# Kernel optimization log

Hardware: AMD Instinct MI355X
Metric: run time of the kernel (lower is better)

## Reference

```python
import jax, jax.numpy as jnp
import numpy as np

BZ, N_STEPS, D_IN, D_HID, D_OUT = 4096, 128, 32, 128, 32


def setup_inputs() -> dict:
    key = jax.random.key(0)
    ks = jax.random.split(key, 16)
    g = lambda k, s: jax.random.normal(k, s, dtype=jnp.float32) * 0.05
    return {
        "fcn_latent": g(ks[0], (BZ, D_IN)),
        "encoder_outputs": g(ks[1], (BZ, N_STEPS, D_HID)),
        "att1_w": g(ks[2], (D_IN, 2 * D_IN)),
        "att1_b": g(ks[3], (D_IN,)),
        "att2_w": g(ks[4], (D_HID, 2 * D_HID)),
        "att2_b": g(ks[5], (D_HID,)),
        "gru1_wih": g(ks[6], (3 * D_HID, D_IN)),
        "gru1_whh": g(ks[7], (3 * D_HID, D_HID)),
        "gru1_bih": g(ks[8], (3 * D_HID,)),
        "gru1_bhh": g(ks[9], (3 * D_HID,)),
        "gru2_wih": g(ks[10], (3 * D_HID, D_HID)),
        "gru2_whh": g(ks[11], (3 * D_HID, D_HID)),
        "gru2_bih": g(ks[12], (3 * D_HID,)),
        "gru2_bhh": g(ks[13], (3 * D_HID,)),
        "out_w": g(ks[14], (D_OUT, D_HID)),
        "out_b": g(ks[15], (D_OUT,)),
    }


def _gru_cell(x, h, w_ih, w_hh, b_ih, b_hh):
    # torch.nn.GRUCell math: gates ordered (r, z, n)
    gi = x @ w_ih.T + b_ih
    gh = h @ w_hh.T + b_hh
    i_r, i_z, i_n = jnp.split(gi, 3, axis=-1)
    h_r, h_z, h_n = jnp.split(gh, 3, axis=-1)
    r = jax.nn.sigmoid(i_r + h_r)
    z = jax.nn.sigmoid(i_z + h_z)
    n = jnp.tanh(i_n + r * h_n)
    return (1.0 - z) * n + z * h


def _attend(h, enc_t, w, b):
    # h: (bz, D), enc_t: (bz, d_enc). Faithful to original (mixes batch into contraction).
    scores = h.T @ enc_t                     # (D, d_enc)
    weight = jax.nn.softmax(scores, axis=-1)
    context = (weight @ enc_t.T).T           # (bz, D)
    return jnp.tanh(jnp.concatenate([context, h], axis=1) @ w.T + b)


def reference(fcn_latent, encoder_outputs, att1_w, att1_b, att2_w, att2_b,
              gru1_wih, gru1_whh, gru1_bih, gru1_bhh,
              gru2_wih, gru2_whh, gru2_bih, gru2_bhh, out_w, out_b):
    # step 0: attention over d_input-sized hidden, then GRUCell(d_input -> d_hidden)
    att0 = _attend(fcn_latent, encoder_outputs[:, 0, :], att1_w, att1_b)
    h_rep = jnp.tile(fcn_latent, (1, D_HID // D_IN))          # (bz, d_hidden)
    h = _gru_cell(att0, h_rep, gru1_wih, gru1_whh, gru1_bih, gru1_bhh)

    def step(h, enc_t):
        a = _attend(h, enc_t, att2_w, att2_b)
        h2 = _gru_cell(a, h, gru2_wih, gru2_whh, gru2_bih, gru2_bhh)
        return h2, h2

    enc_rest = jnp.swapaxes(encoder_outputs[:, 1:, :], 0, 1)  # (n_steps-1, bz, d_hidden)
    _, hs_rest = jax.lax.scan(step, h, enc_rest)
    collector = jnp.concatenate([h[:, None, :], jnp.swapaxes(hs_rest, 0, 1)], axis=1)
    reconstruction = collector @ out_w.T + out_b              # (bz, n_steps, d_output)
    return reconstruction
```

## Files before the change

### kernel.cpp

```cpp
#include <hip/hip_runtime.h>
#include <math.h>

#define BZ 4096
#define NT 128
#define DH 128
#define DI 32
#define LDW 132
#define SCR_KS 2116
#define SA 136
#define ST 40

typedef short bf16x8 __attribute__((ext_vector_type(8)));
typedef float f32x4 __attribute__((ext_vector_type(4)));

__device__ __forceinline__ float4 ld4(const float* p) { return *(const float4*)(p); }
__device__ __forceinline__ void st4(float* p, float4 v) { *(float4*)(p) = v; }
__device__ __forceinline__ float dot4(float4 w, float4 a) {
  return w.x*a.x + w.y*a.y + w.z*a.z + w.w*a.w;
}
__device__ __forceinline__ float sigm(float x) { return 1.f / (1.f + expf(-x)); }
__device__ __forceinline__ unsigned short f2b(float x) {
  unsigned u = __float_as_uint(x);
  u += 0x7FFFu + ((u >> 16) & 1u);
  return (unsigned short)(u >> 16);
}

__global__ __launch_bounds__(512) void k_prep(const float* __restrict__ a2w,
                                              const float* __restrict__ wih,
                                              const float* __restrict__ whh,
                                              const float* __restrict__ outw,
                                              unsigned short* __restrict__ wbf) {
  const int idx = blockIdx.x * 512 + threadIdx.x;
  if (idx >= 147456) return;
  const int tile = idx >> 14, pos = idx & 16383;
  float v;
  if (tile == 0)      v = a2w[(pos >> 7) * 256 + (pos & 127)];
  else if (tile == 1) v = a2w[(pos >> 7) * 256 + 128 + (pos & 127)];
  else if (tile == 2) v = wih[pos];
  else if (tile == 3) v = whh[pos];
  else if (tile == 4) v = wih[16384 + pos];
  else if (tile == 5) v = whh[16384 + pos];
  else if (tile == 6) v = wih[32768 + pos];
  else if (tile == 7) v = whh[32768 + pos];
  else                v = (pos < 4096) ? outw[pos] : 0.f;
  wbf[idx] = f2b(v);
}

template<int D>
__global__ __launch_bounds__(512) void k_scores(const float* __restrict__ hsrc,
                                                const float* __restrict__ enc,
                                                int t, float* __restrict__ spart) {
  constexpr int IG = D / 8;
  constexpr int JC = (D == 128) ? 4 : 1;
  constexpr int HS = D + 4;
  __shared__ float hs[64 * HS];
  __shared__ float es[64 * LDW];
  const int p = blockIdx.x, tid = threadIdx.x, b0 = p * 64;
  for (int idx = tid; idx < 64 * (D / 4); idx += 512) {
    const int r = idx / (D / 4), c4 = (idx % (D / 4)) * 4;
    st4(hs + r * HS + c4, ld4(hsrc + (size_t)(b0 + r) * D + c4));
  }
  for (int idx = tid; idx < 64 * 32; idx += 512) {
    const int r = idx >> 5, c4 = (idx & 31) << 2;
    st4(es + r * LDW + c4, ld4(enc + ((size_t)(b0 + r) * NT + t) * DH + c4));
  }
  __syncthreads();
  const int ig = tid % IG, jg = tid / IG;
  const int i0 = ig * 8, j0 = jg * JC;
  float acc[8][JC];
#pragma unroll
  for (int a = 0; a < 8; ++a)
#pragma unroll
    for (int b = 0; b < JC; ++b) acc[a][b] = 0.f;
  for (int b = 0; b < 64; ++b) {
    float4 h0 = ld4(hs + b * HS + i0);
    float4 h1 = ld4(hs + b * HS + i0 + 4);
    float hv[8] = {h0.x, h0.y, h0.z, h0.w, h1.x, h1.y, h1.z, h1.w};
    float ev[JC];
    if (JC == 4) {
      float4 e = ld4(es + b * LDW + j0);
      ev[0] = e.x; ev[1] = e.y; ev[2] = e.z; ev[3] = e.w;
    } else {
      ev[0] = es[b * LDW + j0];
    }
#pragma unroll
    for (int ii = 0; ii < 8; ++ii)
#pragma unroll
      for (int jj = 0; jj < JC; ++jj) acc[ii][jj] += hv[ii] * ev[jj];
  }
#pragma unroll
  for (int ii = 0; ii < 8; ++ii)
#pragma unroll
    for (int jj = 0; jj < JC; ++jj)
      spart[((size_t)p * D + (i0 + ii)) * 128 + j0 + jj] = acc[ii][jj];
}

template<int R, int P>
__global__ __launch_bounds__(128) void k_soft(const float* __restrict__ spart,
                                              float* __restrict__ W,
                                              unsigned short* __restrict__ Wmb) {
  const int r = blockIdx.x, j = threadIdx.x;
  float s = 0.f;
#pragma unroll 8
  for (int p = 0; p < P; ++p) s += spart[((size_t)p * R + r) * 128 + j];
  __shared__ float xm[2], xs[2];
  float m = s;
  for (int o = 1; o < 64; o <<= 1) m = fmaxf(m, __shfl_xor(m, o));
  if ((j & 63) == 0) xm[j >> 6] = m;
  __syncthreads();
  m = fmaxf(xm[0], xm[1]);
  float e = expf(s - m);
  float sum = e;
  for (int o = 1; o < 64; o <<= 1) sum += __shfl_xor(sum, o);
  if ((j & 63) == 0) xs[j >> 6] = sum;
  __syncthreads();
  sum = xs[0] + xs[1];
  const float val = e / sum;
  W[r * 128 + j] = val;
  Wmb[r * 128 + j] = f2b(val);
}

__global__ __launch_bounds__(128) void k_sum(const float* __restrict__ spart,
                                             float* __restrict__ S1,
                                             float* __restrict__ S2) {
  const int r = blockIdx.x, j = threadIdx.x;
  float s = 0.f;
#pragma unroll 8
  for (int p = 0; p < 64; ++p) s += spart[((size_t)p * 128 + r) * 128 + j];
  S1[r * 128 + j] = s;
  S2[r * 128 + j] = 0.f;
}

struct WTile { bf16x8 k[4]; };
struct AFrag { bf16x8 k[4]; };

__device__ __forceinline__ void loadW(WTile& wt, const unsigned short* __restrict__ base,
                                      int R, int g) {
#pragma unroll
  for (int ks = 0; ks < 4; ++ks)
    wt.k[ks] = *(const bf16x8*)(base + (size_t)R * 128 + ks * 32 + g * 8);
}
__device__ __forceinline__ void loadA(AFrag& a, const unsigned short* act, int n, int g) {
  const char* ab = (const char*)act + n * (2 * SA) + g * 16;
#pragma unroll
  for (int ks = 0; ks < 4; ++ks) a.k[ks] = *(const bf16x8*)(ab + ks * 64);
}
__device__ __forceinline__ void mmrr(f32x4& acc, const AFrag& a, const WTile& w) {
#pragma unroll
  for (int ks = 0; ks < 4; ++ks)
    acc = __builtin_amdgcn_mfma_f32_16x16x32_bf16(a.k[ks], w.k[ks], acc, 0, 0, 0);
}
__device__ __forceinline__ void mmls(f32x4& acc, const unsigned short* Wt,
                                     const unsigned short* act, int R, int n, int g) {
  const char* ab = (const char*)act + n * (2 * SA) + g * 16;
  const char* wb = (const char*)Wt;
  const int sw = (R & 7) << 4;
#pragma unroll
  for (int ks = 0; ks < 4; ++ks) {
    bf16x8 b = *(const bf16x8*)(wb + ((R * 256 + ks * 64 + g * 16) ^ sw));
    bf16x8 a = *(const bf16x8*)(ab + ks * 64);
    acc = __builtin_amdgcn_mfma_f32_16x16x32_bf16(a, b, acc, 0, 0, 0);
  }
}

__global__ __launch_bounds__(512, 2) void k_step3(
    const float* __restrict__ enc, int t, int do_next,
    const float* __restrict__ Srd, float* __restrict__ Sac, float* __restrict__ Szr,
    const unsigned short* __restrict__ wbf,
    const float* __restrict__ att2b,
    const float* __restrict__ bih, const float* __restrict__ bhh,
    float* __restrict__ hist) {
  __shared__ __align__(16) unsigned short Wslot[16384];
  __shared__ __align__(16) unsigned short el[32 * SA], hl[32 * SA];
  __shared__ __align__(16) unsigned short ctxl[32 * SA], al[32 * SA];
  __shared__ __align__(16) unsigned short hnT[128 * ST], encT[128 * ST];
  const int tid = threadIdx.x, b0 = blockIdx.x * 32;
  const int w = tid >> 6, l = tid & 63;
  const int n = l & 15, g4 = l >> 4;
  const int c = w * 16 + n;
  const f32x4 z4 = {0.f, 0.f, 0.f, 0.f};
  const float* __restrict__ hprev_g = hist + (size_t)(t - 1) * (BZ * DH);
  float* __restrict__ hcur_g = hist + (size_t)t * (BZ * DH);

  {
    const int row = tid >> 2, q = tid & 3;
    const float* sr = Srd + row * 128 + q * 32;
    float4 v[8];
    float mx = -1e30f;
#pragma unroll
    for (int i = 0; i < 8; ++i) {
      v[i] = ld4(sr + 4 * i);
      mx = fmaxf(mx, fmaxf(fmaxf(v[i].x, v[i].y), fmaxf(v[i].z, v[i].w)));
    }
    mx = fmaxf(mx, __shfl_xor(mx, 1));
    mx = fmaxf(mx, __shfl_xor(mx, 2));
    float sum = 0.f;
#pragma unroll
    for (int i = 0; i < 8; ++i) {
      v[i].x = expf(v[i].x - mx); v[i].y = expf(v[i].y - mx);
      v[i].z = expf(v[i].z - mx); v[i].w = expf(v[i].w - mx);
      sum += (v[i].x + v[i].y) + (v[i].z + v[i].w);
    }
    sum += __shfl_xor(sum, 1);
    sum += __shfl_xor(sum, 2);
    const float inv = 1.f / sum;
    char* wb = (char*)Wslot;
    const int sw = (row & 7) << 4;
#pragma unroll
    for (int ch = 0; ch < 4; ++ch) {
      unsigned short h8[8] = {
        f2b(v[2*ch].x * inv),   f2b(v[2*ch].y * inv),
        f2b(v[2*ch].z * inv),   f2b(v[2*ch].w * inv),
        f2b(v[2*ch+1].x * inv), f2b(v[2*ch+1].y * inv),
        f2b(v[2*ch+1].z * inv), f2b(v[2*ch+1].w * inv)
      };
      *(uint4*)(wb + ((row * 256 + q * 64 + ch * 16) ^ sw)) = *(const uint4*)h8;
    }
  }

  {
    const int r = tid >> 4, c8 = (tid & 15) << 3;
    float4 e0 = ld4(enc + ((size_t)(b0 + r) * NT + t) * DH + c8);
    float4 e1 = ld4(enc + ((size_t)(b0 + r) * NT + t) * DH + c8 + 4);
    float4 h0 = ld4(hprev_g + (size_t)(b0 + r) * DH + c8);
    float4 h1 = ld4(hprev_g + (size_t)(b0 + r) * DH + c8 + 4);
    unsigned short e8[8] = {f2b(e0.x), f2b(e0.y), f2b(e0.z), f2b(e0.w),
                            f2b(e1.x), f2b(e1.y), f2b(e1.z), f2b(e1.w)};
    unsigned short h8[8] = {f2b(h0.x), f2b(h0.y), f2b(h0.z), f2b(h0.w),
                            f2b(h1.x), f2b(h1.y), f2b(h1.z), f2b(h1.w)};
    *(uint4*)(el + r * SA + c8) = *(const uint4*)e8;
    *(uint4*)(hl + r * SA + c8) = *(const uint4*)h8;
  }
  if (do_next) {
    const int r = tid & 31, c8 = (tid >> 5) << 3;
    float4 e0 = ld4(enc + ((size_t)(b0 + r) * NT + t + 1) * DH + c8);
    float4 e1 = ld4(enc + ((size_t)(b0 + r) * NT + t + 1) * DH + c8 + 4);
    encT[(c8 + 0) * ST + r] = f2b(e0.x); encT[(c8 + 1) * ST + r] = f2b(e0.y);
    encT[(c8 + 2) * ST + r] = f2b(e0.z); encT[(c8 + 3) * ST + r] = f2b(e0.w);
    encT[(c8 + 4) * ST + r] = f2b(e1.x); encT[(c8 + 5) * ST + r] = f2b(e1.y);
    encT[(c8 + 6) * ST + r] = f2b(e1.z); encT[(c8 + 7) * ST + r] = f2b(e1.w);
  }
  if (do_next && tid < 128) Szr[blockIdx.x * 128 + tid] = 0.f;

  WTile wA2a, wA2b, wIR, wHR, wIZ, wHZ, wIN, wHN;
  loadW(wA2a, wbf + 0 * 16384, c, g4);
  loadW(wA2b, wbf + 1 * 16384, c, g4);
  loadW(wIR,  wbf + 2 * 16384, c, g4);
  loadW(wHR,  wbf + 3 * 16384, c, g4);
  loadW(wIZ,  wbf + 4 * 16384, c, g4);
  loadW(wHZ,  wbf + 5 * 16384, c, g4);
  loadW(wIN,  wbf + 6 * 16384, c, g4);
  loadW(wHN,  wbf + 7 * 16384, c, g4);

  float hprev[2][4];
#pragma unroll
  for (int hh = 0; hh < 2; ++hh)
#pragma unroll
    for (int j = 0; j < 4; ++j)
      hprev[hh][j] = hprev_g[(size_t)(b0 + hh * 16 + g4 * 4 + j) * DH + c];
  const float b2c = att2b[c];
  const float bihR = bih[c], bihZ = bih[DH + c], bihN = bih[2 * DH + c];
  const float bhhR = bhh[c], bhhZ = bhh[DH + c], bhhN = bhh[2 * DH + c];
  __syncthreads();

#pragma unroll
  for (int hh = 0; hh < 2; ++hh) {
    f32x4 aC = z4;
    mmls(aC, Wslot, el + hh * 16 * SA, c, n, g4);
#pragma unroll
    for (int j = 0; j < 4; ++j) ctxl[(hh * 16 + g4 * 4 + j) * SA + c] = f2b(aC[j]);
  }
  __syncthreads();
#pragma unroll
  for (int hh = 0; hh < 2; ++hh) {
    AFrag fC, fH;
    loadA(fC, ctxl + hh * 16 * SA, n, g4);
    loadA(fH, hl + hh * 16 * SA, n, g4);
    f32x4 aA = z4;
    mmrr(aA, fC, wA2a);
    mmrr(aA, fH, wA2b);
#pragma unroll
    for (int j = 0; j < 4; ++j)
      al[(hh * 16 + g4 * 4 + j) * SA + c] = f2b(tanhf(aA[j] + b2c));
  }
  __syncthreads();
  f32x4 aR[2], aZ[2], aIN[2], aHN[2];
#pragma unroll
  for (int hh = 0; hh < 2; ++hh) {
    AFrag fA, fH;
    loadA(fA, al + hh * 16 * SA, n, g4);
    loadA(fH, hl + hh * 16 * SA, n, g4);
    f32x4 tr_ = z4, tz = z4, ti = z4, th = z4;
    mmrr(tr_, fA, wIR); mmrr(tr_, fH, wHR);
    mmrr(tz, fA, wIZ);  mmrr(tz, fH, wHZ);
    mmrr(ti, fA, wIN);  mmrr(th, fH, wHN);
    aR[hh] = tr_; aZ[hh] = tz; aIN[hh] = ti; aHN[hh] = th;
  }
#pragma unroll
  for (int hh = 0; hh < 2; ++hh) {
#pragma unroll
    for (int j = 0; j < 4; ++j) {
      const int row = hh * 16 + g4 * 4 + j;
      const float rg = sigm(aR[hh][j] + bihR + bhhR);
      const float zg = sigm(aZ[hh][j] + bihZ + bhhZ);
      const float ng = tanhf(aIN[hh][j] + bihN + rg * (aHN[hh][j] + bhhN));
      const float hv = (1.f - zg) * ng + zg * hprev[hh][j];
      hnT[c * ST + row] = f2b(hv);
      hcur_g[(size_t)(b0 + row) * DH + c] = hv;
    }
  }
  if (!do_next) return;
  __syncthreads();
  {
    bf16x8 afr = *(const bf16x8*)(hnT + (16 * w + n) * ST + g4 * 8);
    float* Sn = Sac + (size_t)(16 * w + g4 * 4) * 128 + n;
#pragma unroll
    for (int nt = 0; nt < 8; ++nt) {
      bf16x8 bfr = *(const bf16x8*)(encT + (16 * nt + n) * ST + g4 * 8);
      f32x4 s = __builtin_amdgcn_mfma_f32_16x16x32_bf16(afr, bfr, z4, 0, 0, 0);
#pragma unroll
      for (int jj = 0; jj < 4; ++jj) atomicAdd(Sn + jj * 128 + nt * 16, s[jj]);
    }
  }
}

__global__ __launch_bounds__(256) void k_out(const float* __restrict__ hist,
                                             const float* __restrict__ outw,
                                             const float* __restrict__ outb,
                                             float* __restrict__ out) {
  __shared__ float wl[32 * 132];
  __shared__ float bl[32];
  const int tid = threadIdx.x;
  for (int idx = tid; idx < 32 * 32; idx += 256) {
    const int r = idx >> 5, c4 = (idx & 31) << 2;
    st4(wl + r * 132 + c4, ld4(outw + r * 128 + c4));
  }
  if (tid < 32) bl[tid] = outb[tid];
  __syncthreads();
  const int rlocal = tid >> 2, q = tid & 3;
  const size_t ri = (size_t)blockIdx.x * 64 + rlocal;
  const int b = (int)(ri & 4095), t = 1 + (int)(ri >> 12);
  const float* hr = hist + (size_t)t * (BZ * DH) + (size_t)b * DH + q * 32;
  float4 hv[8];
#pragma unroll
  for (int i = 0; i < 8; ++i) hv[i] = ld4(hr + 4 * i);
  float acc[32];
#pragma unroll
  for (int o = 0; o < 32; ++o) {
    const float* wr = wl + o * 132 + q * 32;
    float a = 0.f;
#pragma unroll
    for (int i = 0; i < 8; ++i) a += dot4(ld4(wr + 4 * i), hv[i]);
    acc[o] = a;
  }
#pragma unroll
  for (int o = 0; o < 32; ++o) {
    acc[o] += __shfl_xor(acc[o], 1);
    acc[o] += __shfl_xor(acc[o], 2);
  }
  float* op = out + ((size_t)b * NT + t) * DI;
#pragma unroll
  for (int oo = 0; oo < 8; ++oo) {
    const int o = q * 8 + oo;
    op[o] = acc[o] + bl[o];
  }
}

__device__ __forceinline__ void stage128(float* dst, const float* __restrict__ src,
                                         int rows, int srcStride, int tid) {
  const int n4 = rows * 32;
  for (int idx = tid; idx < n4; idx += 512) {
    const int r = idx >> 5, c4 = (idx & 31) << 2;
    st4(dst + r * LDW + c4, ld4(src + (size_t)r * srcStride + c4));
  }
}
template<int ADD>
__device__ __forceinline__ void phase128(float* Wb, const float* act, float* dest, int tid) {
  const int ks = tid & 7, cg_ = (tid >> 3) & 15, r4 = tid >> 7;
  const int rbase = r4 * 4;
  float acc[4][8];
#pragma unroll
  for (int a = 0; a < 4; ++a)
#pragma unroll
    for (int b = 0; b < 8; ++b) acc[a][b] = 0.f;
#pragma unroll
  for (int ch = 0; ch < 4; ++ch) {
    const int k = ks * 4 + ch * 32;
    float4 av[4];
#pragma unroll
    for (int ri = 0; ri < 4; ++ri) av[ri] = ld4(act + (rbase + ri) * LDW + k);
#pragma unroll
    for (int i = 0; i < 8; ++i) {
      float4 wv = ld4(Wb + (cg_ * 8 + i) * LDW + k);
#pragma unroll
      for (int ri = 0; ri < 4; ++ri) acc[ri][i] += dot4(wv, av[ri]);
    }
  }
  __syncthreads();
#pragma unroll
  for (int ri = 0; ri < 4; ++ri) {
    st4(Wb + ks * SCR_KS + (rbase + ri) * LDW + cg_ * 8,
        make_float4(acc[ri][0], acc[ri][1], acc[ri][2], acc[ri][3]));
    st4(Wb + ks * SCR_KS + (rbase + ri) * LDW + cg_ * 8 + 4,
        make_float4(acc[ri][4], acc[ri][5], acc[ri][6], acc[ri][7]));
  }
  __syncthreads();
  const int fr = tid >> 5, fc = (tid & 31) << 2;
  float4 s = make_float4(0.f, 0.f, 0.f, 0.f);
#pragma unroll
  for (int kk = 0; kk < 8; ++kk) {
    float4 v = ld4(Wb + kk * SCR_KS + fr * LDW + fc);
    s.x += v.x; s.y += v.y; s.z += v.z; s.w += v.w;
  }
  float* dp = dest + fr * LDW + fc;
  if (ADD) { float4 o = ld4(dp); s.x += o.x; s.y += o.y; s.z += o.z; s.w += o.w; }
  st4(dp, s);
  __syncthreads();
}
__device__ __forceinline__ void gru_out(float p0, float p1, float p2, float p3,
                                        float bi0, float bi1, float bi2,
                                        float bh0, float bh1, float bh2,
                                        float hv, float* o) {
  const float rg = sigm(p0 + bi0 + bh0);
  const float zg = sigm(p1 + bi1 + bh1);
  const float ng = tanhf(p2 + bi2 + rg * (p3 + bh2));
  *o = (1.f - zg) * ng + zg * hv;
}
__global__ __launch_bounds__(512) void k_main0(
    const float* __restrict__ enc, const float* __restrict__ fcn,
    const float* __restrict__ W0,
    const float* __restrict__ A1, const float* __restrict__ b1,
    const float* __restrict__ wih, const float* __restrict__ whh,
    const float* __restrict__ bih, const float* __restrict__ bhh,
    const float* __restrict__ outw, const float* __restrict__ outb,
    float* __restrict__ h, float* __restrict__ out) {
  __shared__ float Wb[16960];
  __shared__ float el[16 * LDW], hrep[16 * LDW], al[16 * LDW], hn[16 * LDW];
  __shared__ float pre[4][16 * LDW];
  __shared__ float fl[16 * 36];
  const int tid = threadIdx.x, b0 = blockIdx.x * 16;
  {
    const int r = tid >> 5, c4 = (tid & 31) << 2;
    st4(el + r * LDW + c4, ld4(enc + ((size_t)(b0 + r) * NT + 0) * DH + c4));
  }
  {
    const int r = tid >> 5, cc = tid & 31;
    fl[r * 36 + cc] = fcn[(size_t)(b0 + r) * DI + cc];
  }
  __syncthreads();
  {
    const int r = tid >> 5, fc = (tid & 31) << 2;
    st4(hrep + r * LDW + fc, ld4(fl + r * 36 + (fc & 31)));
  }
  stage128(Wb, W0, 32, 128, tid);
  __syncthreads();
  {
    const int r = tid >> 5, q = tid & 31;
    float acc = 0.f;
#pragma unroll 8
    for (int k4 = 0; k4 < 32; ++k4)
      acc += dot4(ld4(Wb + q * LDW + k4 * 4), ld4(el + r * LDW + k4 * 4));
    hn[r * LDW + q] = acc;
  }
  __syncthreads();
  for (int idx = tid; idx < 512; idx += 512) {
    const int r = idx >> 4, c4 = (idx & 15) << 2;
    st4(Wb + r * 68 + c4, ld4(A1 + r * 64 + c4));
  }
  __syncthreads();
  {
    const int r = tid >> 5, i = tid & 31;
    float acc = b1[i];
#pragma unroll
    for (int k4 = 0; k4 < 8; ++k4)
      acc += dot4(ld4(Wb + i * 68 + k4 * 4), ld4(hn + r * LDW + k4 * 4));
#pragma unroll
    for (int k4 = 0; k4 < 8; ++k4)
      acc += dot4(ld4(Wb + i * 68 + 32 + k4 * 4), ld4(fl + r * 36 + k4 * 4));
    al[r * LDW + i] = tanhf(acc);
  }
  __syncthreads();
  for (int idx = tid; idx < 384 * 8; idx += 512) {
    const int r = idx >> 3, c4 = (idx & 7) << 2;
    st4(Wb + r * 36 + c4, ld4(wih + r * 32 + c4));
  }
  __syncthreads();
  {
    const int r = tid >> 5, ccc = tid & 31;
#pragma unroll
    for (int m = 0; m < 12; ++m) {
      const int cc = ccc + 32 * m, g = cc >> 7, col = cc & 127;
      float acc = 0.f;
#pragma unroll
      for (int k4 = 0; k4 < 8; ++k4)
        acc += dot4(ld4(Wb + cc * 36 + k4 * 4), ld4(al + r * LDW + k4 * 4));
      pre[(g == 2) ? 2 : g][r * LDW + col] = acc;
    }
  }
  __syncthreads();
  stage128(Wb, whh, 128, 128, tid);          __syncthreads();
  phase128<1>(Wb, hrep, pre[0], tid);
  stage128(Wb, whh + 16384, 128, 128, tid);  __syncthreads();
  phase128<1>(Wb, hrep, pre[1], tid);
  stage128(Wb, whh + 32768, 128, 128, tid);  __syncthreads();
  phase128<0>(Wb, hrep, pre[3], tid);
  {
    const int fr = tid >> 5, fc = (tid & 31) << 2;
    float4 p0 = ld4(&pre[0][fr * LDW + fc]), p1 = ld4(&pre[1][fr * LDW + fc]);
    float4 p2 = ld4(&pre[2][fr * LDW + fc]), p3 = ld4(&pre[3][fr * LDW + fc]);
    float4 bi0 = ld4(bih + fc), bi1 = ld4(bih + DH + fc), bi2 = ld4(bih + 2 * DH + fc);
    float4 bh0 = ld4(bhh + fc), bh1 = ld4(bhh + DH + fc), bh2 = ld4(bhh + 2 * DH + fc);
    float4 hv = ld4(hrep + fr * LDW + fc);
    float o0, o1, o2, o3;
    gru_out(p0.x, p1.x, p2.x, p3.x, bi0.x, bi1.x, bi2.x, bh0.x, bh1.x, bh2.x, hv.x, &o0);
    gru_out(p0.y, p1.y, p2.y, p3.y, bi0.y, bi1.y, bi2.y, bh0.y, bh1.y, bh2.y, hv.y, &o1);
    gru_out(p0.z, p1.z, p2.z, p3.z, bi0.z, bi1.z, bi2.z, bh0.z, bh1.z, bh2.z, hv.z, &o2);
    gru_out(p0.w, p1.w, p2.w, p3.w, bi0.w, bi1.w, bi2.w, bh0.w, bh1.w, bh2.w, hv.w, &o3);
    float4 hnew = make_float4(o0, o1, o2, o3);
    st4(hn + fr * LDW + fc, hnew);
    st4(h + (size_t)(b0 + fr) * DH + fc, hnew);
  }
  __syncthreads();
  stage128(Wb, outw, 32, 128, tid);
  __syncthreads();
  {
    const int r = tid >> 5, cc = tid & 31;
    float acc = outb[cc];
#pragma unroll 8
    for (int k4 = 0; k4 < 32; ++k4)
      acc += dot4(ld4(Wb + cc * LDW + k4 * 4), ld4(hn + r * LDW + k4 * 4));
    out[((size_t)(b0 + r) * NT + 0) * DI + cc] = acc;
  }
}

extern "C" void kernel_launch(void* const* d_in, const int* in_sizes, int n_in,
                              void* d_out, int out_size, void* d_ws, size_t ws_size,
                              hipStream_t stream) {
  (void)in_sizes; (void)n_in; (void)out_size; (void)ws_size;
  const float* fcn  = (const float*)d_in[0];
  const float* enc  = (const float*)d_in[1];
  const float* a1w  = (const float*)d_in[2];
  const float* a1b  = (const float*)d_in[3];
  const float* a2w  = (const float*)d_in[4];
  const float* a2b  = (const float*)d_in[5];
  const float* w1ih = (const float*)d_in[6];
  const float* w1hh = (const float*)d_in[7];
  const float* b1ih = (const float*)d_in[8];
  const float* b1hh = (const float*)d_in[9];
  const float* w2ih = (const float*)d_in[10];
  const float* w2hh = (const float*)d_in[11];
  const float* b2ih = (const float*)d_in[12];
  const float* b2hh = (const float*)d_in[13];
  const float* outw = (const float*)d_in[14];
  const float* outb = (const float*)d_in[15];
  float* out = (float*)d_out;
  float* ws  = (float*)d_ws;

  float* spart = ws;
  float* Wbuf  = ws + 1048576;
  float* Sbuf  = ws + 1064960;
  unsigned short* wbf = (unsigned short*)(ws + 1130496);
  unsigned short* Wmb = (unsigned short*)(ws + 1204224);
  float* hist  = ws + 1310720;

  k_prep<<<288, 512, 0, stream>>>(a2w, w2ih, w2hh, outw, wbf);

  k_scores<DI><<<64, 512, 0, stream>>>(fcn, enc, 0, spart);
  k_soft<DI, 64><<<DI, 128, 0, stream>>>(spart, Wbuf, Wmb);
  k_main0<<<BZ / 16, 512, 0, stream>>>(enc, fcn, Wbuf, a1w, a1b,
                                       w1ih, w1hh, b1ih, b1hh, outw, outb, hist, out);
  k_scores<DH><<<64, 512, 0, stream>>>(hist, enc, 1, spart);
  k_sum<<<128, 128, 0, stream>>>(spart, Sbuf + 16384, Sbuf + 2 * 16384);

  for (int t = 1; t < NT; ++t) {
    const int do_next = (t < NT - 1) ? 1 : 0;
    const float* Srd = Sbuf + (size_t)(t & 3) * 16384;
    float* Sac = Sbuf + (size_t)((t + 1) & 3) * 16384;
    float* Szr = Sbuf + (size_t)((t + 2) & 3) * 16384;
    k_step3<<<128, 512, 0, stream>>>(enc, t, do_next, Srd, Sac, Szr, wbf, a2b,
                                     b2ih, b2hh, hist);
  }
  k_out<<<(BZ * (NT - 1)) / 64, 256, 0, stream>>>(hist, outw, outb, out);
}
```

Baseline: 3.246 ms.

## Halve step blocks to 64 rows each and fuse output projection into step kernel

```diff
diff --git a/kernel.cpp b/kernel.cpp
--- a/kernel.cpp
+++ b/kernel.cpp
@@ -8,7 +8,7 @@
 #define LDW 132
 #define SCR_KS 2116
 #define SA 136
-#define ST 40
+#define ST2 72
 
 typedef short bf16x8 __attribute__((ext_vector_type(8)));
 typedef float f32x4 __attribute__((ext_vector_type(4)));
@@ -169,12 +169,47 @@
     const unsigned short* __restrict__ wbf,
     const float* __restrict__ att2b,
     const float* __restrict__ bih, const float* __restrict__ bhh,
-    float* __restrict__ hist) {
+    const float* __restrict__ outw, const float* __restrict__ outb,
+    float* __restrict__ hist, float* __restrict__ out) {
   __shared__ __align__(16) unsigned short Wslot[16384];
-  __shared__ __align__(16) unsigned short el[32 * SA], hl[32 * SA];
-  __shared__ __align__(16) unsigned short ctxl[32 * SA], al[32 * SA];
-  __shared__ __align__(16) unsigned short hnT[128 * ST], encT[128 * ST];
-  const int tid = threadIdx.x, b0 = blockIdx.x * 32;
+  __shared__ __align__(16) unsigned short el[64 * SA], hl[64 * SA];
+  __shared__ __align__(16) unsigned short ctxl[64 * SA], al[64 * SA];
+  __shared__ __align__(16) unsigned short hnT[128 * ST2], encT[128 * ST2];
+  const int tid = threadIdx.x;
+
+  if (blockIdx.x >= 64) {
+    if (t < 2) return;
+    const int rl = tid >> 2, q = tid & 3;
+    const int b = (blockIdx.x - 64) * 128 + rl;
+    const int tt = t - 1;
+    const float* hr = hist + (size_t)tt * (BZ * DH) + (size_t)b * DH + q * 32;
+    float4 hv[8];
+#pragma unroll
+    for (int i = 0; i < 8; ++i) hv[i] = ld4(hr + 4 * i);
+    float acc[32];
+#pragma unroll
+    for (int o = 0; o < 32; ++o) {
+      const float* wr = outw + o * 128 + q * 32;
+      float a = 0.f;
+#pragma unroll
+      for (int i = 0; i < 8; ++i) a += dot4(ld4(wr + 4 * i), hv[i]);
+      acc[o] = a;
+    }
+#pragma unroll
+    for (int o = 0; o < 32; ++o) {
+      acc[o] += __shfl_xor(acc[o], 1);
+      acc[o] += __shfl_xor(acc[o], 2);
+    }
+    float* op = out + ((size_t)b * NT + tt) * DI;
+#pragma unroll
+    for (int oo = 0; oo < 8; ++oo) {
+      const int o = q * 8 + oo;
+      op[o] = acc[o] + outb[o];
+    }
+    return;
+  }
+
+  const int b0 = blockIdx.x * 64;
   const int w = tid >> 6, l = tid & 63;
   const int n = l & 15, g4 = l >> 4;
   const int c = w * 16 + n;
@@ -219,28 +254,34 @@
   }
 
   {
-    const int r = tid >> 4, c8 = (tid & 15) << 3;
-    float4 e0 = ld4(enc + ((size_t)(b0 + r) * NT + t) * DH + c8);
-    float4 e1 = ld4(enc + ((size_t)(b0 + r) * NT + t) * DH + c8 + 4);
-    float4 h0 = ld4(hprev_g + (size_t)(b0 + r) * DH + c8);
-    float4 h1 = ld4(hprev_g + (size_t)(b0 + r) * DH + c8 + 4);
-    unsigned short e8[8] = {f2b(e0.x), f2b(e0.y), f2b(e0.z), f2b(e0.w),
-                            f2b(e1.x), f2b(e1.y), f2b(e1.z), f2b(e1.w)};
-    unsigned short h8[8] = {f2b(h0.x), f2b(h0.y), f2b(h0.z), f2b(h0.w),
-                            f2b(h1.x), f2b(h1.y), f2b(h1.z), f2b(h1.w)};
-    *(uint4*)(el + r * SA + c8) = *(const uint4*)e8;
-    *(uint4*)(hl + r * SA + c8) = *(const uint4*)h8;
+    const int r = tid >> 3, cc = (tid & 7) << 4;
+    const float* ep = enc + ((size_t)(b0 + r) * NT + t) * DH + cc;
+    const float* hp = hprev_g + (size_t)(b0 + r) * DH + cc;
+    float4 e0 = ld4(ep), e1 = ld4(ep + 4), e2 = ld4(ep + 8), e3 = ld4(ep + 12);
+    float4 h0 = ld4(hp), h1 = ld4(hp + 4), h2 = ld4(hp + 8), h3 = ld4(hp + 12);
+    unsigned short e8a[8] = {f2b(e0.x), f2b(e0.y), f2b(e0.z), f2b(e0.w),
+                             f2b(e1.x), f2b(e1.y), f2b(e1.z), f2b(e1.w)};
+    unsigned short e8b[8] = {f2b(e2.x), f2b(e2.y), f2b(e2.z), f2b(e2.w),
+                             f2b(e3.x), f2b(e3.y), f2b(e3.z), f2b(e3.w)};
+    unsigned short h8a[8] = {f2b(h0.x), f2b(h0.y), f2b(h0.z), f2b(h0.w),
+                             f2b(h1.x), f2b(h1.y), f2b(h1.z), f2b(h1.w)};
+    unsigned short h8b[8] = {f2b(h2.x), f2b(h2.y), f2b(h2.z), f2b(h2.w),
+                             f2b(h3.x), f2b(h3.y), f2b(h3.z), f2b(h3.w)};
+    *(uint4*)(el + r * SA + cc) = *(const uint4*)e8a;
+    *(uint4*)(el + r * SA + cc + 8) = *(const uint4*)e8b;
+    *(uint4*)(hl + r * SA + cc) = *(const uint4*)h8a;
+    *(uint4*)(hl + r * SA + cc + 8) = *(const uint4*)h8b;
   }
   if (do_next) {
-    const int r = tid & 31, c8 = (tid >> 5) << 3;
-    float4 e0 = ld4(enc + ((size_t)(b0 + r) * NT + t + 1) * DH + c8);
-    float4 e1 = ld4(enc + ((size_t)(b0 + r) * NT + t + 1) * DH + c8 + 4);
-    encT[(c8 + 0) * ST + r] = f2b(e0.x); encT[(c8 + 1) * ST + r] = f2b(e0.y);
-    encT[(c8 + 2) * ST + r] = f2b(e0.z); encT[(c8 + 3) * ST + r] = f2b(e0.w);
-    encT[(c8 + 4) * ST + r] = f2b(e1.x); encT[(c8 + 5) * ST + r] = f2b(e1.y);
-    encT[(c8 + 6) * ST + r] = f2b(e1.z); encT[(c8 + 7) * ST + r] = f2b(e1.w);
-  }
-  if (do_next && tid < 128) Szr[blockIdx.x * 128 + tid] = 0.f;
+    const int r = tid & 63, c16 = (tid >> 6) << 4;
+    const float* ep = enc + ((size_t)(b0 + r) * NT + t + 1) * DH + c16;
+    float4 v0 = ld4(ep), v1 = ld4(ep + 4), v2 = ld4(ep + 8), v3 = ld4(ep + 12);
+    const float vv[16] = {v0.x, v0.y, v0.z, v0.w, v1.x, v1.y, v1.z, v1.w,
+                          v2.x, v2.y, v2.z, v2.w, v3.x, v3.y, v3.z, v3.w};
+#pragma unroll
+    for (int k = 0; k < 16; ++k) encT[(c16 + k) * ST2 + r] = f2b(vv[k]);
+    if (tid < 256) Szr[blockIdx.x * 256 + tid] = 0.f;
+  }
 
   WTile wA2a, wA2b, wIR, wHR, wIZ, wHZ, wIN, wHN;
   loadW(wA2a, wbf + 0 * 16384, c, g4);
@@ -252,9 +293,9 @@
   loadW(wIN,  wbf + 6 * 16384, c, g4);
   loadW(wHN,  wbf + 7 * 16384, c, g4);
 
-  float hprev[2][4];
-#pragma unroll
-  for (int hh = 0; hh < 2; ++hh)
+  float hprev[4][4];
+#pragma unroll
+  for (int hh = 0; hh < 4; ++hh)
 #pragma unroll
     for (int j = 0; j < 4; ++j)
       hprev[hh][j] = hprev_g[(size_t)(b0 + hh * 16 + g4 * 4 + j) * DH + c];
@@ -264,7 +305,7 @@
   __syncthreads();
 
 #pragma unroll
-  for (int hh = 0; hh < 2; ++hh) {
+  for (int hh = 0; hh < 4; ++hh) {
     f32x4 aC = z4;
     mmls(aC, Wslot, el + hh * 16 * SA, c, n, g4);
 #pragma unroll
@@ -272,7 +313,7 @@
   }
   __syncthreads();
 #pragma unroll
-  for (int hh = 0; hh < 2; ++hh) {
+  for (int hh = 0; hh < 4; ++hh) {
     AFrag fC, fH;
     loadA(fC, ctxl + hh * 16 * SA, n, g4);
     loadA(fH, hl + hh * 16 * SA, n, g4);
@@ -284,9 +325,8 @@
       al[(hh * 16 + g4 * 4 + j) * SA + c] = f2b(tanhf(aA[j] + b2c));
   }
   __syncthreads();
-  f32x4 aR[2], aZ[2], aIN[2], aHN[2];
-#pragma unroll
-  for (int hh = 0; hh < 2; ++hh) {
+#pragma unroll
+  for (int hh = 0; hh < 4; ++hh) {
     AFrag fA, fH;
     loadA(fA, al + hh * 16 * SA, n, g4);
     loadA(fH, hl + hh * 16 * SA, n, g4);
@@ -294,30 +334,29 @@
     mmrr(tr_, fA, wIR); mmrr(tr_, fH, wHR);
     mmrr(tz, fA, wIZ);  mmrr(tz, fH, wHZ);
     mmrr(ti, fA, wIN);  mmrr(th, fH, wHN);
-    aR[hh] = tr_; aZ[hh] = tz; aIN[hh] = ti; aHN[hh] = th;
-  }
-#pragma unroll
-  for (int hh = 0; hh < 2; ++hh) {
 #pragma unroll
     for (int j = 0; j < 4; ++j) {
       const int row = hh * 16 + g4 * 4 + j;
-      const float rg = sigm(aR[hh][j] + bihR + bhhR);
-      const float zg = sigm(aZ[hh][j] + bihZ + bhhZ);
-      const float ng = tanhf(aIN[hh][j] + bihN + rg * (aHN[hh][j] + bhhN));
+      const float rg = sigm(tr_[j] + bihR + bhhR);
+      const float zg = sigm(tz[j] + bihZ + bhhZ);
+      const float ng = tanhf(ti[j] + bihN + rg * (th[j] + bhhN));
       const float hv = (1.f - zg) * ng + zg * hprev[hh][j];
-      hnT[c * ST + row] = f2b(hv);
+      hnT[c * ST2 + row] = f2b(hv);
       hcur_g[(size_t)(b0 + row) * DH + c] = hv;
     }
   }
   if (!do_next) return;
   __syncthreads();
   {
-    bf16x8 afr = *(const bf16x8*)(hnT + (16 * w + n) * ST + g4 * 8);
+    bf16x8 afr0 = *(const bf16x8*)(hnT + (16 * w + n) * ST2 + g4 * 8);
+    bf16x8 afr1 = *(const bf16x8*)(hnT + (16 * w + n) * ST2 + 32 + g4 * 8);
     float* Sn = Sac + (size_t)(16 * w + g4 * 4) * 128 + n;
 #pragma unroll
     for (int nt = 0; nt < 8; ++nt) {
-      bf16x8 bfr = *(const bf16x8*)(encT + (16 * nt + n) * ST + g4 * 8);
-      f32x4 s = __builtin_amdgcn_mfma_f32_16x16x32_bf16(afr, bfr, z4, 0, 0, 0);
+      bf16x8 bfr0 = *(const bf16x8*)(encT + (16 * nt + n) * ST2 + g4 * 8);
+      bf16x8 bfr1 = *(const bf16x8*)(encT + (16 * nt + n) * ST2 + 32 + g4 * 8);
+      f32x4 s = __builtin_amdgcn_mfma_f32_16x16x32_bf16(afr0, bfr0, z4, 0, 0, 0);
+      s = __builtin_amdgcn_mfma_f32_16x16x32_bf16(afr1, bfr1, s, 0, 0, 0);
 #pragma unroll
       for (int jj = 0; jj < 4; ++jj) atomicAdd(Sn + jj * 128 + nt * 16, s[jj]);
     }
@@ -327,19 +366,10 @@
 __global__ __launch_bounds__(256) void k_out(const float* __restrict__ hist,
                                              const float* __restrict__ outw,
                                              const float* __restrict__ outb,
-                                             float* __restrict__ out) {
-  __shared__ float wl[32 * 132];
-  __shared__ float bl[32];
+                                             float* __restrict__ out, int t) {
   const int tid = threadIdx.x;
-  for (int idx = tid; idx < 32 * 32; idx += 256) {
-    const int r = idx >> 5, c4 = (idx & 31) << 2;
-    st4(wl + r * 132 + c4, ld4(outw + r * 128 + c4));
-  }
-  if (tid < 32) bl[tid] = outb[tid];
-  __syncthreads();
-  const int rlocal = tid >> 2, q = tid & 3;
-  const size_t ri = (size_t)blockIdx.x * 64 + rlocal;
-  const int b = (int)(ri & 4095), t = 1 + (int)(ri >> 12);
+  const int rl = tid >> 2, q = tid & 3;
+  const int b = blockIdx.x * 64 + rl;
   const float* hr = hist + (size_t)t * (BZ * DH) + (size_t)b * DH + q * 32;
   float4 hv[8];
 #pragma unroll
@@ -347,7 +377,7 @@
   float acc[32];
 #pragma unroll
   for (int o = 0; o < 32; ++o) {
-    const float* wr = wl + o * 132 + q * 32;
+    const float* wr = outw + o * 128 + q * 32;
     float a = 0.f;
 #pragma unroll
     for (int i = 0; i < 8; ++i) a += dot4(ld4(wr + 4 * i), hv[i]);
@@ -362,7 +392,7 @@
 #pragma unroll
   for (int oo = 0; oo < 8; ++oo) {
     const int o = q * 8 + oo;
-    op[o] = acc[o] + bl[o];
+    op[o] = acc[o] + outb[o];
   }
 }
 
@@ -577,8 +607,8 @@
     const float* Srd = Sbuf + (size_t)(t & 3) * 16384;
     float* Sac = Sbuf + (size_t)((t + 1) & 3) * 16384;
     float* Szr = Sbuf + (size_t)((t + 2) & 3) * 16384;
-    k_step3<<<128, 512, 0, stream>>>(enc, t, do_next, Srd, Sac, Szr, wbf, a2b,
-                                     b2ih, b2hh, hist);
-  }
-  k_out<<<(BZ * (NT - 1)) / 64, 256, 0, stream>>>(hist, outw, outb, out);
-}
+    k_step3<<<96, 512, 0, stream>>>(enc, t, do_next, Srd, Sac, Szr, wbf, a2b,
+                                    b2ih, b2hh, outw, outb, hist, out);
+  }
+  k_out<<<64, 256, 0, stream>>>(hist, outw, outb, out, NT - 1);
+}
```

Result: slower. 7.924 ms (+144.1%).

## Overlap output projection with recurrent steps using extra blocks in step kernel

Applied to the files above, without the earlier changes.

```diff
diff --git a/kernel.cpp b/kernel.cpp
--- a/kernel.cpp
+++ b/kernel.cpp
@@ -169,12 +169,47 @@
     const unsigned short* __restrict__ wbf,
     const float* __restrict__ att2b,
     const float* __restrict__ bih, const float* __restrict__ bhh,
-    float* __restrict__ hist) {
+    const float* __restrict__ outw, const float* __restrict__ outb,
+    float* __restrict__ hist, float* __restrict__ out) {
   __shared__ __align__(16) unsigned short Wslot[16384];
   __shared__ __align__(16) unsigned short el[32 * SA], hl[32 * SA];
   __shared__ __align__(16) unsigned short ctxl[32 * SA], al[32 * SA];
   __shared__ __align__(16) unsigned short hnT[128 * ST], encT[128 * ST];
-  const int tid = threadIdx.x, b0 = blockIdx.x * 32;
+  const int tid = threadIdx.x;
+
+  if (blockIdx.x >= 128) {
+    if (t < 2) return;
+    const int rl = tid >> 2, q = tid & 3;
+    const int b = (blockIdx.x - 128) * 128 + rl;
+    const int tt = t - 1;
+    const float* hr = hist + (size_t)tt * (BZ * DH) + (size_t)b * DH + q * 32;
+    float4 hv[8];
+#pragma unroll
+    for (int i = 0; i < 8; ++i) hv[i] = ld4(hr + 4 * i);
+    float acc[32];
+#pragma unroll
+    for (int o = 0; o < 32; ++o) {
+      const float* wr = outw + o * 128 + q * 32;
+      float a = 0.f;
+#pragma unroll
+      for (int i = 0; i < 8; ++i) a += dot4(ld4(wr + 4 * i), hv[i]);
+      acc[o] = a;
+    }
+#pragma unroll
+    for (int o = 0; o < 32; ++o) {
+      acc[o] += __shfl_xor(acc[o], 1);
+      acc[o] += __shfl_xor(acc[o], 2);
+    }
+    float* op = out + ((size_t)b * NT + tt) * DI;
+#pragma unroll
+    for (int oo = 0; oo < 8; ++oo) {
+      const int o = q * 8 + oo;
+      op[o] = acc[o] + outb[o];
+    }
+    return;
+  }
+
+  const int b0 = blockIdx.x * 32;
   const int w = tid >> 6, l = tid & 63;
   const int n = l & 15, g4 = l >> 4;
   const int c = w * 16 + n;
@@ -327,19 +362,10 @@
 __global__ __launch_bounds__(256) void k_out(const float* __restrict__ hist,
                                              const float* __restrict__ outw,
                                              const float* __restrict__ outb,
-                                             float* __restrict__ out) {
-  __shared__ float wl[32 * 132];
-  __shared__ float bl[32];
+                                             float* __restrict__ out, int t) {
   const int tid = threadIdx.x;
-  for (int idx = tid; idx < 32 * 32; idx += 256) {
-    const int r = idx >> 5, c4 = (idx & 31) << 2;
-    st4(wl + r * 132 + c4, ld4(outw + r * 128 + c4));
-  }
-  if (tid < 32) bl[tid] = outb[tid];
-  __syncthreads();
-  const int rlocal = tid >> 2, q = tid & 3;
-  const size_t ri = (size_t)blockIdx.x * 64 + rlocal;
-  const int b = (int)(ri & 4095), t = 1 + (int)(ri >> 12);
+  const int rl = tid >> 2, q = tid & 3;
+  const int b = blockIdx.x * 64 + rl;
   const float* hr = hist + (size_t)t * (BZ * DH) + (size_t)b * DH + q * 32;
   float4 hv[8];
 #pragma unroll
@@ -347,7 +373,7 @@
   float acc[32];
 #pragma unroll
   for (int o = 0; o < 32; ++o) {
-    const float* wr = wl + o * 132 + q * 32;
+    const float* wr = outw + o * 128 + q * 32;
     float a = 0.f;
 #pragma unroll
     for (int i = 0; i < 8; ++i) a += dot4(ld4(wr + 4 * i), hv[i]);
@@ -362,7 +388,7 @@
 #pragma unroll
   for (int oo = 0; oo < 8; ++oo) {
     const int o = q * 8 + oo;
-    op[o] = acc[o] + bl[o];
+    op[o] = acc[o] + outb[o];
   }
 }
 
@@ -577,8 +603,8 @@
     const float* Srd = Sbuf + (size_t)(t & 3) * 16384;
     float* Sac = Sbuf + (size_t)((t + 1) & 3) * 16384;
     float* Szr = Sbuf + (size_t)((t + 2) & 3) * 16384;
-    k_step3<<<128, 512, 0, stream>>>(enc, t, do_next, Srd, Sac, Szr, wbf, a2b,
-                                     b2ih, b2hh, hist);
-  }
-  k_out<<<(BZ * (NT - 1)) / 64, 256, 0, stream>>>(hist, outw, outb, out);
-}
+    k_step3<<<160, 512, 0, stream>>>(enc, t, do_next, Srd, Sac, Szr, wbf, a2b,
+                                     b2ih, b2hh, outw, outb, hist, out);
+  }
+  k_out<<<64, 256, 0, stream>>>(hist, outw, outb, out, NT - 1);
+}
```

Measured after the change: 7.946 ms. 2.45x slower.
